# Kernel optimization log

Hardware: AMD Instinct MI355X
Metric: run time of the kernel (lower is better)

Reference implementation:

```python
import jax, jax.numpy as jnp
import numpy as np

NUM_SUBSPACES = 8
CODEBOOK_SIZE = 256
SUBSPACE_DIM = 96


def setup_inputs() -> dict:
    key = jax.random.key(0)
    k1, k2 = jax.random.split(key)
    embeddings = jax.random.normal(k1, (16, 4096, NUM_SUBSPACES * SUBSPACE_DIM), dtype=jnp.float32)
    codebooks = jax.random.normal(k2, (NUM_SUBSPACES, CODEBOOK_SIZE, SUBSPACE_DIM), dtype=jnp.float32)
    return {"embeddings": embeddings, "codebooks": codebooks}


def reference(embeddings, codebooks):
    # embeddings: [B, S, E] with E = M*d; codebooks: [M, K, d]
    B, S, E = embeddings.shape
    M, K, d = codebooks.shape
    # [N, M, d] -> [M, N, d] so each subspace is contiguous
    x = embeddings.reshape(B * S, M, d).transpose(1, 0, 2)
    x2 = jnp.sum(x * x, axis=-1, keepdims=True)              # [M, N, 1]
    c2 = jnp.sum(codebooks * codebooks, axis=-1)[:, None, :]  # [M, 1, K]
    xc = jnp.einsum('mnd,mkd->mnk', x, codebooks)             # [M, N, K]
    dist2 = x2 - 2.0 * xc + c2                                # [M, N, K]
    # argmin over codes (same result as cdist p=2 argmin since sqrt is monotone)
    idx = jnp.argmin(dist2, axis=-1)                          # [M, N]
    # gather nearest codewords per subspace
    quantized = codebooks[jnp.arange(M)[:, None], idx]        # [M, N, d]
    # reassemble: [N, M, d] -> [B, S, E]
    return quantized.transpose(1, 0, 2).reshape(B, S, E)
```

## Files before the change

kernel.cpp:

```cpp
#include <hip/hip_runtime.h>

typedef short   bf16x8 __attribute__((ext_vector_type(8)));
typedef unsigned short u16x4 __attribute__((ext_vector_type(4)));
typedef unsigned short u16x8 __attribute__((ext_vector_type(8)));
typedef float   f32x16 __attribute__((ext_vector_type(16)));

constexpr int NSUB  = 8;
constexpr int NCODE = 256;
constexpr int SDIM  = 96;
constexpr int EMB   = NSUB * SDIM;
constexpr int TILE_ROWS = 64;
constexpr int ROWS_PER_BLK = 512;
constexpr int NTILES = ROWS_PER_BLK / TILE_ROWS;
constexpr float C_SHIFT = 192.0f;
constexpr float THR = 0.02f;

constexpr int    CB_UNITS      = 8 * 6 * 2 * 64;
constexpr size_t WS_FRAG_BYTES = (size_t)NSUB * CB_UNITS * 16;
constexpr size_t WS_NEEDED     = WS_FRAG_BYTES + (size_t)NSUB * NCODE * 4;

constexpr int X_OFF     = 0;
constexpr int C2_OFF    = X_OFF + 24576;
constexpr int SB_OFF    = C2_OFF + 1024;
constexpr int BK_OFF    = SB_OFF + 4096;
constexpr int LDS_TOTAL = BK_OFF + 256;

__device__ __forceinline__ unsigned short f2bf(float v) {
    unsigned u = __builtin_bit_cast(unsigned, v);
    u = u + 0x7FFFu + ((u >> 16) & 1u);
    return (unsigned short)(u >> 16);
}
__device__ __forceinline__ float bf2f(unsigned short h) {
    unsigned u = ((unsigned)h) << 16;
    return __builtin_bit_cast(float, u);
}

__device__ __forceinline__ int xaddr(int u, int off) {
    return u * 1024 + (off ^ ((u & 7) << 4));
}

__device__ __forceinline__ void gll4(const void* g, void* lds) {
    __builtin_amdgcn_global_load_lds((const __attribute__((address_space(1))) unsigned int*)g,
                                     (__attribute__((address_space(3))) unsigned int*)lds, 4, 0, 0);
}

__global__ __launch_bounds__(256) void pq_prep(const float* __restrict__ cb,
                                               unsigned short* __restrict__ wsf,
                                               float* __restrict__ wsc2)
{
    const int m   = (int)blockIdx.x;
    const int tid = (int)threadIdx.x;
    {
        const float* c = cb + ((size_t)m * NCODE + tid) * SDIM;
        double s = 0.0;
        for (int k = 0; k < SDIM; ++k) { double v = (double)c[k]; s += v * v; }
        wsc2[m * NCODE + tid] = (float)(0.5 * s + (double)C_SHIFT);
    }
    for (int i = 0; i < 24; ++i) {
        int u  = i * 256 + tid;
        int l  = u & 63;
        int c6 = u >> 6;
        int h  = c6 & 1; c6 >>= 1;
        int s  = c6 % 6;
        int t  = c6 / 6;
        int code = t * 32 + (l & 31);
        int k0   = s * 16 + (l >> 5) * 8;
        const float* src = cb + (size_t)m * NCODE * SDIM + (size_t)code * SDIM + k0;
        u16x8 o;
        #pragma unroll
        for (int j = 0; j < 8; ++j) {
            float v = -src[j];
            unsigned short hb = f2bf(v);
            o[j] = (h == 0) ? hb : f2bf(v - bf2f(hb));
        }
        *(u16x8*)(wsf + ((size_t)m * CB_UNITS + u) * 8) = o;
    }
}

__global__ __launch_bounds__(512) void pq_mfma7(
    const float* __restrict__ emb,
    const float* __restrict__ cb,
    const unsigned short* __restrict__ wsf,
    const float* __restrict__ wsc2,
    float* __restrict__ out,
    int nrows)
{
    extern __shared__ char smem[];
    const int tid   = (int)threadIdx.x;
    const int w     = tid >> 6;
    const int lane  = tid & 63;
    const int hib   = lane >> 5;
    const int g     = w & 1;
    const int tq    = w >> 1;
    const int m     = (int)(blockIdx.x & 7);
    const int chunk = (int)(blockIdx.x >> 3);
    const int row0  = chunk * ROWS_PER_BLK;

    float4* sb = (float4*)(smem + SB_OFF);
    int*    bk = (int*)(smem + BK_OFF);

    const unsigned short* wb = wsf + (size_t)m * CB_UNITS * 8;

    if (w < 4) gll4(wsc2 + m * NCODE + w * 64 + lane, smem + C2_OFF + w * 256);

    float4 xf[3];
    auto issue_x = [&](int t) {
        #pragma unroll
        for (int ii = 0; ii < 3; ++ii) {
            int Q = ii * 512 + tid;
            int r = Q / 24, f = Q % 24;
            int gr = row0 + t * TILE_ROWS + r;
            if (gr >= nrows) gr = nrows - 1;
            xf[ii] = *(const float4*)(emb + (size_t)gr * EMB + m * SDIM + f * 4);
        }
    };
    auto convert_x = [&]() {
        #pragma unroll
        for (int ii = 0; ii < 3; ++ii) {
            int Q = ii * 512 + tid;
            int r = Q / 24, f = Q % 24;
            int s = f >> 2, kh = (f >> 1) & 1, j0 = f & 1;
            int g2 = r >> 5, lp = (r & 31) + 32 * kh;
            float v[4] = { xf[ii].x, xf[ii].y, xf[ii].z, xf[ii].w };
            u16x4 hi4, lo4;
            #pragma unroll
            for (int e = 0; e < 4; ++e) {
                unsigned short hb = f2bf(v[e]);
                hi4[e] = hb;
                lo4[e] = f2bf(v[e] - bf2f(hb));
            }
            int uh  = (g2 * 6 + s) * 2;
            int off = lp * 16 + j0 * 8;
            *(u16x4*)(smem + X_OFF + xaddr(uh, off))     = hi4;
            *(u16x4*)(smem + X_OFF + xaddr(uh + 1, off)) = lo4;
        }
    };

    issue_x(0);
    convert_x();
    issue_x(1);
    __syncthreads();

    #pragma unroll 1
    for (int t = 0; t < NTILES; ++t) {
        const int rowt0 = row0 + t * TILE_ROWS;

        const int t0 = tq * 2, t1 = t0 + 1;
        f32x16 a0, a1;
        {
            const float* c2p = (const float*)(smem + C2_OFF);
            #pragma unroll
            for (int rq = 0; rq < 4; ++rq) {
                float4 q0 = *(const float4*)(c2p + t0 * 32 + rq * 8 + hib * 4);
                float4 q1 = *(const float4*)(c2p + t1 * 32 + rq * 8 + hib * 4);
                a0[rq*4+0]=q0.x; a0[rq*4+1]=q0.y; a0[rq*4+2]=q0.z; a0[rq*4+3]=q0.w;
                a1[rq*4+0]=q1.x; a1[rq*4+1]=q1.y; a1[rq*4+2]=q1.z; a1[rq*4+3]=q1.w;
            }
        }
        {
            const char* xbp = smem + X_OFF;
            #pragma unroll
            for (int s = 0; s < 6; ++s) {
                bf16x8 xh  = *(const bf16x8*)(xbp + xaddr((g * 6 + s) * 2,     lane * 16));
                bf16x8 xl  = *(const bf16x8*)(xbp + xaddr((g * 6 + s) * 2 + 1, lane * 16));
                bf16x8 ah0 = *(const bf16x8*)(wb + (size_t)((((t0 * 6 + s) * 2) + 0) * 64 + lane) * 8);
                bf16x8 al0 = *(const bf16x8*)(wb + (size_t)((((t0 * 6 + s) * 2) + 1) * 64 + lane) * 8);
                bf16x8 ah1 = *(const bf16x8*)(wb + (size_t)((((t1 * 6 + s) * 2) + 0) * 64 + lane) * 8);
                bf16x8 al1 = *(const bf16x8*)(wb + (size_t)((((t1 * 6 + s) * 2) + 1) * 64 + lane) * 8);
                a0 = __builtin_amdgcn_mfma_f32_32x32x16_bf16(ah0, xh, a0, 0, 0, 0);
                a1 = __builtin_amdgcn_mfma_f32_32x32x16_bf16(ah1, xh, a1, 0, 0, 0);
                a0 = __builtin_amdgcn_mfma_f32_32x32x16_bf16(al0, xh, a0, 0, 0, 0);
                a1 = __builtin_amdgcn_mfma_f32_32x32x16_bf16(al1, xh, a1, 0, 0, 0);
                a0 = __builtin_amdgcn_mfma_f32_32x32x16_bf16(ah0, xl, a0, 0, 0, 0);
                a1 = __builtin_amdgcn_mfma_f32_32x32x16_bf16(ah1, xl, a1, 0, 0, 0);
            }
        }
        float b1 = 3.4e38f, b2 = 3.4e38f;
        int   i1 = 1 << 30, i2 = 1 << 30;
        #pragma unroll
        for (int r = 0; r < 16; ++r) {
            float sv = a0[r];
            int   kv = t0 * 32 + (r & 3) + 8 * (r >> 2) + hib * 4;
            if (sv < b1)      { b2 = b1; i2 = i1; b1 = sv; i1 = kv; }
            else if (sv < b2) { b2 = sv; i2 = kv; }
        }
        #pragma unroll
        for (int r = 0; r < 16; ++r) {
            float sv = a1[r];
            int   kv = t1 * 32 + (r & 3) + 8 * (r >> 2) + hib * 4;
            if (sv < b1)      { b2 = b1; i2 = i1; b1 = sv; i1 = kv; }
            else if (sv < b2) { b2 = sv; i2 = kv; }
        }
        {
            float ob1 = __shfl_xor(b1, 32);
            int   oi1 = __shfl_xor(i1, 32);
            float ob2 = __shfl_xor(b2, 32);
            int   oi2 = __shfl_xor(i2, 32);
            bool o1_better = (ob1 < b1) || (ob1 == b1 && oi1 < i1);
            if (o1_better) {
                bool mine_better = (b1 < ob2) || (b1 == ob2 && i1 < oi2);
                if (mine_better) { b2 = b1; i2 = i1; } else { b2 = ob2; i2 = oi2; }
                b1 = ob1; i1 = oi1;
            } else {
                if ((ob1 < b2) || (ob1 == b2 && oi1 < i2)) { b2 = ob1; i2 = oi1; }
            }
        }
        if (lane < 32)
            sb[tq * TILE_ROWS + g * 32 + lane] =
                make_float4(b1, b2, __builtin_bit_cast(float, i1), __builtin_bit_cast(float, i2));
        __syncthreads();

        if (tid < TILE_ROWS) {
            int r = tid;
            float4 A = sb[r];
            float mb1 = A.x, mb2 = A.y;
            int   mi1 = __builtin_bit_cast(int, A.z), mi2 = __builtin_bit_cast(int, A.w);
            #pragma unroll
            for (int q = 1; q < 4; ++q) {
                float4 B = sb[q * TILE_ROWS + r];
                float q1 = B.x, q2 = B.y;
                int   qi1 = __builtin_bit_cast(int, B.z), qi2 = __builtin_bit_cast(int, B.w);
                if (q1 < mb1)      { mb2 = mb1; mi2 = mi1; mb1 = q1; mi1 = qi1; }
                else if (q1 < mb2) { mb2 = q1;  mi2 = qi1; }
                if (q2 < mb2)      { mb2 = q2;  mi2 = qi2; }
            }
            int grow = rowt0 + r;
            if (grow < nrows) {
                if (mb2 - mb1 < THR) {
                    const float* xr = emb + (size_t)grow * EMB + m * SDIM;
                    const float* ca = cb + ((size_t)m * NCODE + mi1) * SDIM;
                    const float* cbv = cb + ((size_t)m * NCODE + mi2) * SDIM;
                    double da = 0.0, db = 0.0;
                    for (int kk = 0; kk < SDIM; ++kk) {
                        double ea = (double)xr[kk] - (double)ca[kk];
                        double eb = (double)xr[kk] - (double)cbv[kk];
                        da += ea * ea; db += eb * eb;
                    }
                    if (db < da || (db == da && mi2 < mi1)) mi1 = mi2;
                }
                bk[r] = mi1;
            }
        }
        __syncthreads();

        if (t + 1 < NTILES) { convert_x(); issue_x(t + 2); }
        {
            #pragma unroll
            for (int ii = 0; ii < 3; ++ii) {
                int Q = ii * 512 + tid;
                int r = Q / 24, f = Q % 24;
                int grow = rowt0 + r;
                if (grow < nrows) {
                    int k = bk[r];
                    float4 v = *(const float4*)(cb + ((size_t)m * NCODE + k) * SDIM + f * 4);
                    *(float4*)(out + (size_t)grow * EMB + m * SDIM + f * 4) = v;
                }
            }
        }
        __syncthreads();
    }
}

__global__ __launch_bounds__(256) void pq_argmin_kernel(
    const float* __restrict__ emb, const float* __restrict__ cb,
    float* __restrict__ out, int nrows)
{
    const int m   = (int)(blockIdx.x & 7);
    const int row = (int)(blockIdx.x >> 3) * 256 + (int)threadIdx.x;
    const float* __restrict__ cbm = cb + (size_t)m * (NCODE * SDIM);
    __shared__ float half_c2[NCODE];
    {
        const int k = (int)threadIdx.x;
        const float* c = cbm + k * SDIM;
        float s = 0.f;
        #pragma unroll
        for (int i = 0; i < SDIM; i += 4) {
            const float4 v = *reinterpret_cast<const float4*>(c + i);
            s = fmaf(v.x, v.x, s); s = fmaf(v.y, v.y, s);
            s = fmaf(v.z, v.z, s); s = fmaf(v.w, v.w, s);
        }
        half_c2[k] = 0.5f * s;
    }
    __syncthreads();
    if (row >= nrows) return;
    float x[SDIM];
    {
        const float* xr = emb + (size_t)row * EMB + m * SDIM;
        #pragma unroll
        for (int i = 0; i < SDIM; i += 4) {
            const float4 v = *reinterpret_cast<const float4*>(xr + i);
            x[i+0] = v.x; x[i+1] = v.y; x[i+2] = v.z; x[i+3] = v.w;
        }
    }
    float best = 3.4e38f, best2 = 3.4e38f;
    int bestk = 0, bestk2 = 0;
    #pragma unroll 1
    for (int k = 0; k < NCODE; k += 4) {
        const float* c0 = cbm + (k + 0) * SDIM;
        const float* c1 = cbm + (k + 1) * SDIM;
        const float* c2 = cbm + (k + 2) * SDIM;
        const float* c3 = cbm + (k + 3) * SDIM;
        float a0 = 0.f, a1 = 0.f, a2 = 0.f, a3 = 0.f;
        #pragma unroll
        for (int i = 0; i < SDIM; i += 4) {
            const float4 v0 = *reinterpret_cast<const float4*>(c0 + i);
            const float4 v1 = *reinterpret_cast<const float4*>(c1 + i);
            const float4 v2 = *reinterpret_cast<const float4*>(c2 + i);
            const float4 v3 = *reinterpret_cast<const float4*>(c3 + i);
            a0 = fmaf(x[i+0], v0.x, a0); a0 = fmaf(x[i+1], v0.y, a0);
            a0 = fmaf(x[i+2], v0.z, a0); a0 = fmaf(x[i+3], v0.w, a0);
            a1 = fmaf(x[i+0], v1.x, a1); a1 = fmaf(x[i+1], v1.y, a1);
            a1 = fmaf(x[i+2], v1.z, a1); a1 = fmaf(x[i+3], v1.w, a1);
            a2 = fmaf(x[i+0], v2.x, a2); a2 = fmaf(x[i+1], v2.y, a2);
            a2 = fmaf(x[i+2], v2.z, a2); a2 = fmaf(x[i+3], v2.w, a2);
            a3 = fmaf(x[i+0], v3.x, a3); a3 = fmaf(x[i+1], v3.y, a3);
            a3 = fmaf(x[i+2], v3.z, a3); a3 = fmaf(x[i+3], v3.w, a3);
        }
        const float s[4] = { half_c2[k+0] - a0, half_c2[k+1] - a1,
                             half_c2[k+2] - a2, half_c2[k+3] - a3 };
        #pragma unroll
        for (int j = 0; j < 4; ++j) {
            if (s[j] < best)       { best2 = best; bestk2 = bestk; best = s[j]; bestk = k + j; }
            else if (s[j] < best2) { best2 = s[j]; bestk2 = k + j; }
        }
    }
    if (best2 - best < 0.02f) {
        const float* ca = cbm + bestk  * SDIM;
        const float* cbv = cbm + bestk2 * SDIM;
        double da = 0.0, db = 0.0;
        for (int i = 0; i < SDIM; ++i) {
            const double ea = (double)x[i] - (double)ca[i];
            const double eb = (double)x[i] - (double)cbv[i];
            da += ea * ea; db += eb * eb;
        }
        if (db < da || (db == da && bestk2 < bestk)) bestk = bestk2;
    }
    const float* cbest = cbm + bestk * SDIM;
    float* o = out + (size_t)row * EMB + m * SDIM;
    #pragma unroll
    for (int i = 0; i < SDIM; i += 4)
        *reinterpret_cast<float4*>(o + i) = *reinterpret_cast<const float4*>(cbest + i);
}

extern "C" void kernel_launch(void* const* d_in, const int* in_sizes, int n_in,
                              void* d_out, int out_size, void* d_ws, size_t ws_size,
                              hipStream_t stream) {
    const float* emb = (const float*)d_in[0];
    const float* cb  = (const float*)d_in[1];
    float* out = (float*)d_out;
    const int nrows = in_sizes[0] / EMB;

    if (ws_size < WS_NEEDED) {
        const int rowBlocks = (nrows + 255) / 256;
        pq_argmin_kernel<<<dim3(rowBlocks * NSUB), dim3(256), 0, stream>>>(emb, cb, out, nrows);
        return;
    }

    unsigned short* wsf = (unsigned short*)d_ws;
    float* wsc2 = (float*)((char*)d_ws + WS_FRAG_BYTES);

    pq_prep<<<dim3(NSUB), dim3(256), 0, stream>>>(cb, wsf, wsc2);

    hipFuncSetAttribute((const void*)pq_mfma7,
                        hipFuncAttributeMaxDynamicSharedMemorySize, LDS_TOTAL);
    const int nb = (nrows + ROWS_PER_BLK - 1) / ROWS_PER_BLK;
    pq_mfma7<<<dim3(nb * NSUB), dim3(512), LDS_TOTAL, stream>>>(
        emb, cb, wsf, wsc2, out, nrows);
}
```

Before: 236.7 us.

## Restructure PQ kernel to one wave per 32 rows over all codes, no LDS

Replaces the 512-thread block kernel, which tiles 64 rows across 8 waves with LDS staging, cross-wave reductions and barriers, with a wave-independent kernel. Each wave loads and splits its 32 rows into bf16 hi/lo registers and loops over all 256 codes. It keeps the top-2 candidates in registers, resolves the final index with a single lane shuffle, and then gathers the output. This removes LDS traffic, __syncthreads and the cross-wave merge, but every wave now streams the whole codebook fragments from global/L2 and loses the software prefetch of x.

After: 206.2 us. 1.15x faster.

```diff
diff --git a/kernel.cpp b/kernel.cpp
--- a/kernel.cpp
+++ b/kernel.cpp
@@ -1,7 +1,6 @@
 #include <hip/hip_runtime.h>
 
 typedef short   bf16x8 __attribute__((ext_vector_type(8)));
-typedef unsigned short u16x4 __attribute__((ext_vector_type(4)));
 typedef unsigned short u16x8 __attribute__((ext_vector_type(8)));
 typedef float   f32x16 __attribute__((ext_vector_type(16)));
 
@@ -9,21 +8,12 @@
 constexpr int NCODE = 256;
 constexpr int SDIM  = 96;
 constexpr int EMB   = NSUB * SDIM;
-constexpr int TILE_ROWS = 64;
-constexpr int ROWS_PER_BLK = 512;
-constexpr int NTILES = ROWS_PER_BLK / TILE_ROWS;
 constexpr float C_SHIFT = 192.0f;
 constexpr float THR = 0.02f;
 
 constexpr int    CB_UNITS      = 8 * 6 * 2 * 64;
 constexpr size_t WS_FRAG_BYTES = (size_t)NSUB * CB_UNITS * 16;
 constexpr size_t WS_NEEDED     = WS_FRAG_BYTES + (size_t)NSUB * NCODE * 4;
-
-constexpr int X_OFF     = 0;
-constexpr int C2_OFF    = X_OFF + 24576;
-constexpr int SB_OFF    = C2_OFF + 1024;
-constexpr int BK_OFF    = SB_OFF + 4096;
-constexpr int LDS_TOTAL = BK_OFF + 256;
 
 __device__ __forceinline__ unsigned short f2bf(float v) {
     unsigned u = __builtin_bit_cast(unsigned, v);
@@ -33,15 +23,6 @@
 __device__ __forceinline__ float bf2f(unsigned short h) {
     unsigned u = ((unsigned)h) << 16;
     return __builtin_bit_cast(float, u);
-}
-
-__device__ __forceinline__ int xaddr(int u, int off) {
-    return u * 1024 + (off ^ ((u & 7) << 4));
-}
-
-__device__ __forceinline__ void gll4(const void* g, void* lds) {
-    __builtin_amdgcn_global_load_lds((const __attribute__((address_space(1))) unsigned int*)g,
-                                     (__attribute__((address_space(3))) unsigned int*)lds, 4, 0, 0);
 }
 
 __global__ __launch_bounds__(256) void pq_prep(const float* __restrict__ cb,
@@ -77,106 +58,72 @@
     }
 }
 
-__global__ __launch_bounds__(512) void pq_mfma7(
+__global__ __launch_bounds__(256, 3) void pq_mfma8(
     const float* __restrict__ emb,
     const float* __restrict__ cb,
     const unsigned short* __restrict__ wsf,
     const float* __restrict__ wsc2,
     float* __restrict__ out,
-    int nrows)
+    int nrows,
+    int rowblks)
 {
-    extern __shared__ char smem[];
-    const int tid   = (int)threadIdx.x;
-    const int w     = tid >> 6;
-    const int lane  = tid & 63;
-    const int hib   = lane >> 5;
-    const int g     = w & 1;
-    const int tq    = w >> 1;
-    const int m     = (int)(blockIdx.x & 7);
-    const int chunk = (int)(blockIdx.x >> 3);
-    const int row0  = chunk * ROWS_PER_BLK;
-
-    float4* sb = (float4*)(smem + SB_OFF);
-    int*    bk = (int*)(smem + BK_OFF);
+    const int tid  = (int)threadIdx.x;
+    const int lane = tid & 63;
+    const int hib  = lane >> 5;
+    const int widx = (int)blockIdx.x * 4 + (tid >> 6);
+    if (widx >= NSUB * rowblks) return;
+    const int m    = widx / rowblks;
+    const int rb   = widx % rowblks;
+    const int row0 = rb * 32;
 
     const unsigned short* wb = wsf + (size_t)m * CB_UNITS * 8;
-
-    if (w < 4) gll4(wsc2 + m * NCODE + w * 64 + lane, smem + C2_OFF + w * 256);
-
-    float4 xf[3];
-    auto issue_x = [&](int t) {
-        #pragma unroll
-        for (int ii = 0; ii < 3; ++ii) {
-            int Q = ii * 512 + tid;
-            int r = Q / 24, f = Q % 24;
-            int gr = row0 + t * TILE_ROWS + r;
-            if (gr >= nrows) gr = nrows - 1;
-            xf[ii] = *(const float4*)(emb + (size_t)gr * EMB + m * SDIM + f * 4);
-        }
-    };
-    auto convert_x = [&]() {
-        #pragma unroll
-        for (int ii = 0; ii < 3; ++ii) {
-            int Q = ii * 512 + tid;
-            int r = Q / 24, f = Q % 24;
-            int s = f >> 2, kh = (f >> 1) & 1, j0 = f & 1;
-            int g2 = r >> 5, lp = (r & 31) + 32 * kh;
-            float v[4] = { xf[ii].x, xf[ii].y, xf[ii].z, xf[ii].w };
-            u16x4 hi4, lo4;
+    const float* c2p = wsc2 + m * NCODE;
+
+    bf16x8 xh[6], xl[6];
+    {
+        int r = row0 + (lane & 31);
+        if (r >= nrows) r = nrows - 1;
+        const float* xr = emb + (size_t)r * EMB + m * SDIM + hib * 8;
+        #pragma unroll
+        for (int s = 0; s < 6; ++s) {
+            float4 v0 = *(const float4*)(xr + s * 16);
+            float4 v1 = *(const float4*)(xr + s * 16 + 4);
+            float v[8] = { v0.x, v0.y, v0.z, v0.w, v1.x, v1.y, v1.z, v1.w };
             #pragma unroll
-            for (int e = 0; e < 4; ++e) {
-                unsigned short hb = f2bf(v[e]);
-                hi4[e] = hb;
-                lo4[e] = f2bf(v[e] - bf2f(hb));
+            for (int j = 0; j < 8; ++j) {
+                unsigned short hb = f2bf(v[j]);
+                xh[s][j] = (short)hb;
+                xl[s][j] = (short)f2bf(v[j] - bf2f(hb));
             }
-            int uh  = (g2 * 6 + s) * 2;
-            int off = lp * 16 + j0 * 8;
-            *(u16x4*)(smem + X_OFF + xaddr(uh, off))     = hi4;
-            *(u16x4*)(smem + X_OFF + xaddr(uh + 1, off)) = lo4;
-        }
-    };
-
-    issue_x(0);
-    convert_x();
-    issue_x(1);
-    __syncthreads();
-
+        }
+    }
+
+    float b1 = 3.4e38f, b2 = 3.4e38f;
+    int   i1 = 1 << 30, i2 = 1 << 30;
     #pragma unroll 1
-    for (int t = 0; t < NTILES; ++t) {
-        const int rowt0 = row0 + t * TILE_ROWS;
-
-        const int t0 = tq * 2, t1 = t0 + 1;
+    for (int p = 0; p < 4; ++p) {
+        const int t0 = p * 2, t1 = t0 + 1;
         f32x16 a0, a1;
-        {
-            const float* c2p = (const float*)(smem + C2_OFF);
-            #pragma unroll
-            for (int rq = 0; rq < 4; ++rq) {
-                float4 q0 = *(const float4*)(c2p + t0 * 32 + rq * 8 + hib * 4);
-                float4 q1 = *(const float4*)(c2p + t1 * 32 + rq * 8 + hib * 4);
-                a0[rq*4+0]=q0.x; a0[rq*4+1]=q0.y; a0[rq*4+2]=q0.z; a0[rq*4+3]=q0.w;
-                a1[rq*4+0]=q1.x; a1[rq*4+1]=q1.y; a1[rq*4+2]=q1.z; a1[rq*4+3]=q1.w;
-            }
-        }
-        {
-            const char* xbp = smem + X_OFF;
-            #pragma unroll
-            for (int s = 0; s < 6; ++s) {
-                bf16x8 xh  = *(const bf16x8*)(xbp + xaddr((g * 6 + s) * 2,     lane * 16));
-                bf16x8 xl  = *(const bf16x8*)(xbp + xaddr((g * 6 + s) * 2 + 1, lane * 16));
-                bf16x8 ah0 = *(const bf16x8*)(wb + (size_t)((((t0 * 6 + s) * 2) + 0) * 64 + lane) * 8);
-                bf16x8 al0 = *(const bf16x8*)(wb + (size_t)((((t0 * 6 + s) * 2) + 1) * 64 + lane) * 8);
-                bf16x8 ah1 = *(const bf16x8*)(wb + (size_t)((((t1 * 6 + s) * 2) + 0) * 64 + lane) * 8);
-                bf16x8 al1 = *(const bf16x8*)(wb + (size_t)((((t1 * 6 + s) * 2) + 1) * 64 + lane) * 8);
-                a0 = __builtin_amdgcn_mfma_f32_32x32x16_bf16(ah0, xh, a0, 0, 0, 0);
-                a1 = __builtin_amdgcn_mfma_f32_32x32x16_bf16(ah1, xh, a1, 0, 0, 0);
-                a0 = __builtin_amdgcn_mfma_f32_32x32x16_bf16(al0, xh, a0, 0, 0, 0);
-                a1 = __builtin_amdgcn_mfma_f32_32x32x16_bf16(al1, xh, a1, 0, 0, 0);
-                a0 = __builtin_amdgcn_mfma_f32_32x32x16_bf16(ah0, xl, a0, 0, 0, 0);
-                a1 = __builtin_amdgcn_mfma_f32_32x32x16_bf16(ah1, xl, a1, 0, 0, 0);
-            }
-        }
-        float b1 = 3.4e38f, b2 = 3.4e38f;
-        int   i1 = 1 << 30, i2 = 1 << 30;
+        #pragma unroll
+        for (int rq = 0; rq < 4; ++rq) {
+            float4 q0 = *(const float4*)(c2p + t0 * 32 + rq * 8 + hib * 4);
+            float4 q1 = *(const float4*)(c2p + t1 * 32 + rq * 8 + hib * 4);
+            a0[rq*4+0]=q0.x; a0[rq*4+1]=q0.y; a0[rq*4+2]=q0.z; a0[rq*4+3]=q0.w;
+            a1[rq*4+0]=q1.x; a1[rq*4+1]=q1.y; a1[rq*4+2]=q1.z; a1[rq*4+3]=q1.w;
+        }
+        #pragma unroll
+        for (int s = 0; s < 6; ++s) {
+            bf16x8 ah0 = *(const bf16x8*)(wb + (size_t)((((t0 * 6 + s) * 2) + 0) * 64 + lane) * 8);
+            bf16x8 al0 = *(const bf16x8*)(wb + (size_t)((((t0 * 6 + s) * 2) + 1) * 64 + lane) * 8);
+            bf16x8 ah1 = *(const bf16x8*)(wb + (size_t)((((t1 * 6 + s) * 2) + 0) * 64 + lane) * 8);
+            bf16x8 al1 = *(const bf16x8*)(wb + (size_t)((((t1 * 6 + s) * 2) + 1) * 64 + lane) * 8);
+            a0 = __builtin_amdgcn_mfma_f32_32x32x16_bf16(ah0, xh[s], a0, 0, 0, 0);
+            a1 = __builtin_amdgcn_mfma_f32_32x32x16_bf16(ah1, xh[s], a1, 0, 0, 0);
+            a0 = __builtin_amdgcn_mfma_f32_32x32x16_bf16(al0, xh[s], a0, 0, 0, 0);
+            a1 = __builtin_amdgcn_mfma_f32_32x32x16_bf16(al1, xh[s], a1, 0, 0, 0);
+            a0 = __builtin_amdgcn_mfma_f32_32x32x16_bf16(ah0, xl[s], a0, 0, 0, 0);
+            a1 = __builtin_amdgcn_mfma_f32_32x32x16_bf16(ah1, xl[s], a1, 0, 0, 0);
+        }
         #pragma unroll
         for (int r = 0; r < 16; ++r) {
             float sv = a0[r];
@@ -191,73 +138,48 @@
             if (sv < b1)      { b2 = b1; i2 = i1; b1 = sv; i1 = kv; }
             else if (sv < b2) { b2 = sv; i2 = kv; }
         }
-        {
-            float ob1 = __shfl_xor(b1, 32);
-            int   oi1 = __shfl_xor(i1, 32);
-            float ob2 = __shfl_xor(b2, 32);
-            int   oi2 = __shfl_xor(i2, 32);
-            bool o1_better = (ob1 < b1) || (ob1 == b1 && oi1 < i1);
-            if (o1_better) {
-                bool mine_better = (b1 < ob2) || (b1 == ob2 && i1 < oi2);
-                if (mine_better) { b2 = b1; i2 = i1; } else { b2 = ob2; i2 = oi2; }
-                b1 = ob1; i1 = oi1;
-            } else {
-                if ((ob1 < b2) || (ob1 == b2 && oi1 < i2)) { b2 = ob1; i2 = oi1; }
+    }
+    {
+        float ob1 = __shfl_xor(b1, 32);
+        int   oi1 = __shfl_xor(i1, 32);
+        float ob2 = __shfl_xor(b2, 32);
+        int   oi2 = __shfl_xor(i2, 32);
+        bool o1_better = (ob1 < b1) || (ob1 == b1 && oi1 < i1);
+        if (o1_better) {
+            bool mine_better = (b1 < ob2) || (b1 == ob2 && i1 < oi2);
+            if (mine_better) { b2 = b1; i2 = i1; } else { b2 = ob2; i2 = oi2; }
+            b1 = ob1; i1 = oi1;
+        } else {
+            if ((ob1 < b2) || (ob1 == b2 && oi1 < i2)) { b2 = ob1; i2 = oi1; }
+        }
+    }
+
+    {
+        int grow = row0 + (lane & 31);
+        if (lane < 32 && grow < nrows && (b2 - b1 < THR)) {
+            const float* xr = emb + (size_t)grow * EMB + m * SDIM;
+            const float* ca = cb + ((size_t)m * NCODE + i1) * SDIM;
+            const float* cbv = cb + ((size_t)m * NCODE + i2) * SDIM;
+            double da = 0.0, db = 0.0;
+            for (int kk = 0; kk < SDIM; ++kk) {
+                double ea = (double)xr[kk] - (double)ca[kk];
+                double eb = (double)xr[kk] - (double)cbv[kk];
+                da += ea * ea; db += eb * eb;
             }
-        }
-        if (lane < 32)
-            sb[tq * TILE_ROWS + g * 32 + lane] =
-                make_float4(b1, b2, __builtin_bit_cast(float, i1), __builtin_bit_cast(float, i2));
-        __syncthreads();
-
-        if (tid < TILE_ROWS) {
-            int r = tid;
-            float4 A = sb[r];
-            float mb1 = A.x, mb2 = A.y;
-            int   mi1 = __builtin_bit_cast(int, A.z), mi2 = __builtin_bit_cast(int, A.w);
-            #pragma unroll
-            for (int q = 1; q < 4; ++q) {
-                float4 B = sb[q * TILE_ROWS + r];
-                float q1 = B.x, q2 = B.y;
-                int   qi1 = __builtin_bit_cast(int, B.z), qi2 = __builtin_bit_cast(int, B.w);
-                if (q1 < mb1)      { mb2 = mb1; mi2 = mi1; mb1 = q1; mi1 = qi1; }
-                else if (q1 < mb2) { mb2 = q1;  mi2 = qi1; }
-                if (q2 < mb2)      { mb2 = q2;  mi2 = qi2; }
-            }
-            int grow = rowt0 + r;
-            if (grow < nrows) {
-                if (mb2 - mb1 < THR) {
-                    const float* xr = emb + (size_t)grow * EMB + m * SDIM;
-                    const float* ca = cb + ((size_t)m * NCODE + mi1) * SDIM;
-                    const float* cbv = cb + ((size_t)m * NCODE + mi2) * SDIM;
-                    double da = 0.0, db = 0.0;
-                    for (int kk = 0; kk < SDIM; ++kk) {
-                        double ea = (double)xr[kk] - (double)ca[kk];
-                        double eb = (double)xr[kk] - (double)cbv[kk];
-                        da += ea * ea; db += eb * eb;
-                    }
-                    if (db < da || (db == da && mi2 < mi1)) mi1 = mi2;
-                }
-                bk[r] = mi1;
-            }
-        }
-        __syncthreads();
-
-        if (t + 1 < NTILES) { convert_x(); issue_x(t + 2); }
-        {
-            #pragma unroll
-            for (int ii = 0; ii < 3; ++ii) {
-                int Q = ii * 512 + tid;
-                int r = Q / 24, f = Q % 24;
-                int grow = rowt0 + r;
-                if (grow < nrows) {
-                    int k = bk[r];
-                    float4 v = *(const float4*)(cb + ((size_t)m * NCODE + k) * SDIM + f * 4);
-                    *(float4*)(out + (size_t)grow * EMB + m * SDIM + f * 4) = v;
-                }
-            }
-        }
-        __syncthreads();
+            if (db < da || (db == da && i2 < i1)) i1 = i2;
+        }
+    }
+
+    #pragma unroll
+    for (int ii = 0; ii < 12; ++ii) {
+        int Q = ii * 64 + lane;
+        int r = Q / 24, f = Q % 24;
+        int grow = row0 + r;
+        int k = __shfl(i1, r);
+        if (grow < nrows) {
+            float4 v = *(const float4*)(cb + ((size_t)m * NCODE + k) * SDIM + f * 4);
+            *(float4*)(out + (size_t)grow * EMB + m * SDIM + f * 4) = v;
+        }
     }
 }
 
@@ -361,9 +283,8 @@
 
     pq_prep<<<dim3(NSUB), dim3(256), 0, stream>>>(cb, wsf, wsc2);
 
-    hipFuncSetAttribute((const void*)pq_mfma7,
-                        hipFuncAttributeMaxDynamicSharedMemorySize, LDS_TOTAL);
-    const int nb = (nrows + ROWS_PER_BLK - 1) / ROWS_PER_BLK;
-    pq_mfma7<<<dim3(nb * NSUB), dim3(512), LDS_TOTAL, stream>>>(
-        emb, cb, wsf, wsc2, out, nrows);
-}
+    const int rowblks = (nrows + 31) / 32;
+    const int nwaves  = rowblks * NSUB;
+    const int nb      = (nwaves + 3) / 4;
+    pq_mfma8<<<dim3(nb), dim3(256), 0, stream>>>(emb, cb, wsf, wsc2, out, nrows, rowblks);
+}
```
